# Kernel optimization log

Hardware: AMD Instinct MI355X
Metric: run time of the kernel (lower is better)

Reference implementation:

```python
import jax, jax.numpy as jnp
import numpy as np

MARGIN = 0.075
CONF_THRESHOLD = 0.2


def setup_inputs() -> dict:
    key = jax.random.key(0)
    k1, k2, k3 = jax.random.split(key, 3)
    N, D = 32768, 256
    embeddings = jax.random.normal(k1, (N, D), dtype=jnp.float32)
    tags = jax.random.randint(k2, (N,), 0, 500, dtype=jnp.int64)
    confidences = jax.random.uniform(k3, (N,), dtype=jnp.float32)
    return {"embeddings": embeddings, "tags": tags, "confidences": confidences}


def _safe_sqrt(sq):
    # gradient-safe sqrt: zero at sq<=0 (matches d(0)=0, avoids NaN in vjp)
    pos = sq > 0
    return jnp.where(pos, jnp.sqrt(jnp.where(pos, sq, 1.0)), 0.0)


def _triplet_hard_mining(emb, labels):
    n = emb.shape[0]
    # pairwise euclidean distances (cdist p=2)
    sq_norm = jnp.sum(emb * emb, axis=1)  # [n]
    sq = sq_norm[:, None] + sq_norm[None, :] - 2.0 * (emb @ emb.T)
    dist = _safe_sqrt(jnp.maximum(sq, 0.0))  # [n, n]

    same = labels[:, None] == labels[None, :]
    eye = jnp.eye(n, dtype=bool)
    pos_mask = same & ~eye
    neg_mask = ~same

    inf = jnp.float32(jnp.inf)
    hard_pos = jnp.max(jnp.where(pos_mask, dist, -inf), axis=1)  # [n]
    neg_min = jnp.min(jnp.where(neg_mask, dist, inf), axis=1)    # [n]
    # semi-hard negatives: neg dists strictly greater than hardest positive
    shn_mask = neg_mask & (dist > hard_pos[:, None])
    shn_min = jnp.min(jnp.where(shn_mask, dist, inf), axis=1)
    hard_neg = jnp.where(jnp.isfinite(shn_min), shn_min, neg_min)

    valid = jnp.any(pos_mask, axis=1) & jnp.any(neg_mask, axis=1)
    per_anchor = jax.nn.relu(hard_pos - hard_neg + MARGIN)
    per_anchor = jnp.where(valid, per_anchor, 0.0)
    cnt = jnp.sum(valid.astype(jnp.float32))
    # if no valid anchors (also covers <2 unique labels), loss is 0
    return jnp.where(cnt > 0, jnp.sum(per_anchor) / jnp.maximum(cnt, 1.0), 0.0)


def reference(embeddings, tags, confidences):
    n = embeddings.shape[0]
    top_k = int(CONF_THRESHOLD * n)
    _, idx = jax.lax.top_k(confidences, top_k)
    emb = embeddings[idx]
    labels = tags[idx]
    return _triplet_hard_mining(emb, labels)
```

## Files before the change

### kernel.cpp

```cpp
#include <hip/hip_runtime.h>
#include <math.h>

#define D 256
#define MARGIN 0.075f
#define MAXM 96

typedef __bf16 bf8_t __attribute__((ext_vector_type(8)));
typedef float f4_t __attribute__((ext_vector_type(4)));
typedef unsigned long long ull;

#define AS1 __attribute__((address_space(1)))
#define AS3 __attribute__((address_space(3)))
static __device__ __forceinline__ void gload_lds16(const void* g, void* s) {
    __builtin_amdgcn_global_load_lds((const AS1 unsigned int*)g, (AS3 unsigned int*)s, 16, 0, 0);
}

static __device__ __forceinline__ unsigned short f2bf(float x) {
    unsigned u = __float_as_uint(x);
    unsigned r = (u + 0x7fffu + ((u >> 16) & 1u)) >> 16;
    return (unsigned short)r;
}

static __device__ __forceinline__ float dec_min(unsigned cm) {
    return (cm == 0u) ? __builtin_inff() : __uint_as_float(~cm);
}

static __device__ __forceinline__ float rmin16(float v) {
    int s;
    s = __builtin_amdgcn_update_dpp(__float_as_int(v), __float_as_int(v), 0x101, 0xF, 0xF, false);
    v = fminf(v, __int_as_float(s));
    s = __builtin_amdgcn_update_dpp(__float_as_int(v), __float_as_int(v), 0x102, 0xF, 0xF, false);
    v = fminf(v, __int_as_float(s));
    s = __builtin_amdgcn_update_dpp(__float_as_int(v), __float_as_int(v), 0x104, 0xF, 0xF, false);
    v = fminf(v, __int_as_float(s));
    s = __builtin_amdgcn_update_dpp(__float_as_int(v), __float_as_int(v), 0x108, 0xF, 0xF, false);
    v = fminf(v, __int_as_float(s));
    return v;
}

__global__ void k_hist1(const float* __restrict__ conf, int n,
                        unsigned* __restrict__ hist) {
    int i = blockIdx.x * blockDim.x + threadIdx.x;
    if (i < n) atomicAdd(&hist[__float_as_uint(conf[i]) >> 16], 1u);
}

__global__ __launch_bounds__(1024) void k_scan(const unsigned* __restrict__ hist,
                                               unsigned* __restrict__ ctrl, int ksel) {
    __shared__ unsigned part[1024];
    __shared__ int schunk;
    int t = threadIdx.x;
    unsigned k = (unsigned)ksel;
    unsigned s = 0;
    const uint4* h4 = (const uint4*)(hist + t * 64);
    #pragma unroll
    for (int b = 0; b < 16; b++) { uint4 v = h4[b]; s += v.x + v.y + v.z + v.w; }
    part[t] = s;
    __syncthreads();
    for (int off = 1; off < 1024; off <<= 1) {
        unsigned v = (t + off < 1024) ? part[t + off] : 0u;
        __syncthreads();
        part[t] += v;
        __syncthreads();
    }
    if (part[t] >= k && (t == 1023 || part[t + 1] < k)) schunk = t;
    __syncthreads();
    if (t == 0) {
        int c = schunk;
        unsigned cum = (c == 1023) ? 0u : part[c + 1];
        int bin = 0; unsigned rem = 1;
        for (int b = 63; b >= 0; b--) {
            unsigned h = hist[c * 64 + b];
            if (cum + h >= k) { bin = c * 64 + b; rem = k - cum; break; }
            cum += h;
        }
        ctrl[3] = (unsigned)bin;
        ctrl[1] = k - rem;
        ctrl[2] = rem;
    }
}

__global__ void k_sel(const float* __restrict__ conf, int n,
                      unsigned* __restrict__ ctrl, int* __restrict__ idx_sel,
                      ull* __restrict__ cand) {
    int i = blockIdx.x * blockDim.x + threadIdx.x;
    if (i < n) {
        unsigned u = __float_as_uint(conf[i]);
        unsigned t16 = u >> 16, b16 = ctrl[3];
        if (t16 > b16) {
            unsigned pos = atomicAdd(&ctrl[5], 1u);
            idx_sel[pos] = i;
        } else if (t16 == b16) {
            unsigned pos = atomicAdd(&ctrl[6], 1u);
            cand[pos] = ((ull)u << 32) | (unsigned)i;
        }
    }
}

__global__ __launch_bounds__(256) void k_sel2(const unsigned* __restrict__ ctrl,
                                              const ull* __restrict__ cand,
                                              int* __restrict__ idx_sel) {
    int t = threadIdx.x;
    int M = (int)ctrl[6];
    unsigned need = ctrl[2], cgt = ctrl[1];
    for (int j = t; j < M; j += 256) {
        ull cj = cand[j];
        unsigned uj = (unsigned)(cj >> 32);
        unsigned rank = 0;
        for (int m = 0; m < M; m++) {
            ull cm = cand[m];
            unsigned um = (unsigned)(cm >> 32);
            if (um > uj || (um == uj && cm < cj)) rank++;
        }
        if (rank < need) idx_sel[cgt + rank] = (int)(unsigned)(cj & 0xFFFFFFFFu);
    }
}

__global__ void k_gather(const float* __restrict__ emb, const int* __restrict__ tags,
                         const int* __restrict__ idx_sel, int ksel, int np,
                         unsigned short* __restrict__ ebf, float* __restrict__ sqn,
                         int* __restrict__ lsel, unsigned* __restrict__ labhist,
                         int* __restrict__ members) {
    int j = blockIdx.x;
    int t = threadIdx.x;
    if (j < ksel) {
        int src = idx_sel[j];
        float4 v = *(const float4*)&emb[(size_t)src * D + t * 4];
        ushort4 o;
        o.x = f2bf(v.x); o.y = f2bf(v.y); o.z = f2bf(v.z); o.w = f2bf(v.w);
        *(ushort4*)&ebf[(size_t)j * D + t * 4] = o;
        float s = v.x * v.x + v.y * v.y + v.z * v.z + v.w * v.w;
        for (int off = 32; off > 0; off >>= 1) s += __shfl_down(s, off);
        if (t == 0) {
            int lab = tags[src];
            sqn[j] = s; lsel[j] = lab;
            unsigned slot = atomicAdd(&labhist[lab], 1u);
            if (slot < MAXM) members[lab * MAXM + slot] = j;
        }
    } else {
        ushort4 z = {0, 0, 0, 0};
        *(ushort4*)&ebf[(size_t)j * D + t * 4] = z;
        if (t == 0) { sqn[j] = 0.f; lsel[j] = -1; }
    }
}

__global__ __launch_bounds__(256) void k_hardpos(const unsigned short* __restrict__ ebf,
                                                 const float* __restrict__ sqn,
                                                 const int* __restrict__ members,
                                                 const unsigned* __restrict__ labhist,
                                                 unsigned* __restrict__ hp_g) {
    int L = blockIdx.x;
    int t = threadIdx.x;
    int m = (int)labhist[L];
    if (m > MAXM) m = MAXM;
    if (m < 2) return;

    __shared__ unsigned short rows[MAXM * 256];
    __shared__ float lsqn[MAXM];
    __shared__ unsigned hpl[MAXM];
    __shared__ int ridx[MAXM];

    for (int a = t; a < m; a += 256) {
        int r = members[L * MAXM + a];
        ridx[a] = r; lsqn[a] = sqn[r]; hpl[a] = 0u;
    }
    __syncthreads();
    for (int e = t * 8; e < m * 256; e += 256 * 8) {
        int a = e >> 8, c = e & 255;
        *(uint4*)&rows[a * 256 + c] = *(const uint4*)&ebf[(size_t)ridx[a] * D + c];
    }
    __syncthreads();

    int npair = m * (m - 1) / 2;
    for (int pidx = t; pidx < npair; pidx += 256) {
        int a = 0, rem = pidx;
        while (rem >= m - 1 - a) { rem -= m - 1 - a; a++; }
        int b = a + 1 + rem;
        const unsigned* ra = (const unsigned*)&rows[a * 256];
        const unsigned* rb = (const unsigned*)&rows[b * 256];
        float dot = 0.f;
        #pragma unroll 8
        for (int c = 0; c < 128; c++) {
            unsigned ua = ra[c], ub = rb[c];
            float a0 = __uint_as_float(ua << 16);
            float a1 = __uint_as_float(ua & 0xFFFF0000u);
            float b0 = __uint_as_float(ub << 16);
            float b1 = __uint_as_float(ub & 0xFFFF0000u);
            dot = fmaf(a0, b0, dot);
            dot = fmaf(a1, b1, dot);
        }
        float dsq = fmaxf(lsqn[a] + lsqn[b] - 2.f * dot, 0.f);
        unsigned bits = __float_as_uint(dsq);
        atomicMax(&hpl[a], bits);
        atomicMax(&hpl[b], bits);
    }
    __syncthreads();
    for (int a = t; a < m; a += 256) hp_g[ridx[a]] = hpl[a];
}

__global__ __launch_bounds__(256, 3) void k_fused(const unsigned short* __restrict__ Ebf,
                                                  const float* __restrict__ sqn,
                                                  const int* __restrict__ lsel,
                                                  const unsigned* __restrict__ hp_g,
                                                  unsigned* __restrict__ nm_g,
                                                  unsigned* __restrict__ shn_g,
                                                  int np, int nb, int ksel) {
    int rem = blockIdx.x, bi = 0;
    while (rem >= nb - bi) { rem -= nb - bi; bi++; }
    int bj = bi + rem;
    int i0 = bi * 128, j0 = bj * 128;
    bool diag = (bi == bj);

    __shared__ __align__(16) char smem[32768];
    char* ldsA = smem;
    char* ldsB = smem + 16384;

    int t = threadIdx.x;
    int w = t >> 6, l = t & 63;
    int wm = w & 1, wn = w >> 1;
    int lr = l & 15, lq = l >> 4;
    int r7 = lr & 7, rh = lr >> 3;

    int dr = l >> 3;
    int sg = (l & 7) ^ dr;
    const unsigned short* gA = Ebf + (size_t)(i0 + dr) * D + sg * 8;
    const unsigned short* gB = Ebf + (size_t)(j0 + dr) * D + sg * 8;

    f4_t zero = {0.f, 0.f, 0.f, 0.f};
    f4_t acc[4][4];
    #pragma unroll
    for (int p = 0; p < 4; p++)
        #pragma unroll
        for (int q = 0; q < 4; q++) acc[p][q] = zero;

    for (int k0 = 0; k0 < D; k0 += 64) {
        #pragma unroll
        for (int c = 0; c < 4; c++) {
            int R0 = w * 32 + c * 8;
            gload_lds16(gA + (size_t)R0 * D + k0, ldsA + R0 * 128);
            gload_lds16(gB + (size_t)R0 * D + k0, ldsB + R0 * 128);
        }
        __syncthreads();
        #pragma unroll
        for (int ks8 = 0; ks8 < 8; ks8 += 4) {
            bf8_t a[4], b[4];
            #pragma unroll
            for (int p = 0; p < 4; p++) {
                int off = ((wm * 8 + p * 2 + rh) << 10) + ((r7 * 8 + ((ks8 + lq) ^ r7)) << 4);
                a[p] = *(const bf8_t*)(ldsA + off);
            }
            #pragma unroll
            for (int q = 0; q < 4; q++) {
                int off = ((wn * 8 + q * 2 + rh) << 10) + ((r7 * 8 + ((ks8 + lq) ^ r7)) << 4);
                b[q] = *(const bf8_t*)(ldsB + off);
            }
            #pragma unroll
            for (int p = 0; p < 4; p++)
                #pragma unroll
                for (int q = 0; q < 4; q++)
                    acc[p][q] = __builtin_amdgcn_mfma_f32_16x16x32_bf16(a[p], b[q], acc[p][q], 0, 0, 0);
        }
        __syncthreads();
    }

    float* sqnA = (float*)smem;
    float* sqnB = sqnA + 128;
    int* labA = (int*)(sqnB + 128);
    int* labB = labA + 128;
    float* hpA2 = (float*)(labB + 128);
    float* hpB2 = hpA2 + 128;
    if (t < 128) {
        sqnA[t] = sqn[i0 + t];
        labA[t] = lsel[i0 + t];
        hpA2[t] = __uint_as_float(hp_g[i0 + t]);
    } else {
        int u = t - 128;
        sqnB[u] = sqn[j0 + u];
        labB[u] = lsel[j0 + u];
        hpB2[u] = __uint_as_float(hp_g[j0 + u]);
    }
    __syncthreads();

    const float INF = __builtin_inff();
    float dsq[4][4][4];
    int colL[4], ljv[4];
    #pragma unroll
    for (int q = 0; q < 4; q++) { colL[q] = wn * 64 + q * 16 + lr; ljv[q] = labB[colL[q]]; }
    #pragma unroll
    for (int p = 0; p < 4; p++) {
        #pragma unroll
        for (int r = 0; r < 4; r++) {
            int rowL = wm * 64 + p * 16 + lq * 4 + r;
            int gm = i0 + rowL;
            float smi = sqnA[rowL];
            #pragma unroll
            for (int q = 0; q < 4; q++) {
                int gn = j0 + colL[q];
                float s = fmaxf(smi + sqnB[colL[q]] - 2.f * acc[p][q][r], 0.f);
                dsq[p][q][r] = (gm < ksel && gn < ksel) ? s : INF;
            }
        }
    }

    #pragma unroll
    for (int p = 0; p < 4; p++) {
        #pragma unroll
        for (int r = 0; r < 4; r++) {
            int rowL = wm * 64 + p * 16 + lq * 4 + r;
            int li = labA[rowL];
            float hpr = hpA2[rowL];
            float nmv = INF, smv = INF;
            #pragma unroll
            for (int q = 0; q < 4; q++) {
                float d = dsq[p][q][r];
                if (ljv[q] != li) {
                    nmv = fminf(nmv, d);
                    if (d > hpr) smv = fminf(smv, d);
                }
            }
            nmv = rmin16(nmv);
            smv = rmin16(smv);
            if (lr == 0) {
                if (nmv < INF) atomicMax(&nm_g[i0 + rowL], ~__float_as_uint(nmv));
                if (smv < INF) atomicMax(&shn_g[i0 + rowL], ~__float_as_uint(smv));
            }
        }
    }

    if (!diag) {
        #pragma unroll
        for (int q = 0; q < 4; q++) {
            int lj = ljv[q];
            float hpc = hpB2[colL[q]];
            float nmv = INF, smv = INF;
            #pragma unroll
            for (int p = 0; p < 4; p++)
                #pragma unroll
                for (int r = 0; r < 4; r++) {
                    int rowL = wm * 64 + p * 16 + lq * 4 + r;
                    float d = dsq[p][q][r];
                    if (labA[rowL] != lj) {
                        nmv = fminf(nmv, d);
                        if (d > hpc) smv = fminf(smv, d);
                    }
                }
            nmv = fminf(nmv, __shfl_xor(nmv, 16));
            nmv = fminf(nmv, __shfl_xor(nmv, 32));
            smv = fminf(smv, __shfl_xor(smv, 16));
            smv = fminf(smv, __shfl_xor(smv, 32));
            if (lq == 0) {
                if (nmv < INF) atomicMax(&nm_g[j0 + colL[q]], ~__float_as_uint(nmv));
                if (smv < INF) atomicMax(&shn_g[j0 + colL[q]], ~__float_as_uint(smv));
            }
        }
    }
}

__global__ __launch_bounds__(256) void k_loss(const unsigned* __restrict__ hp,
                                              const unsigned* __restrict__ nm,
                                              const unsigned* __restrict__ shn,
                                              const int* __restrict__ lsel,
                                              const unsigned* __restrict__ labhist,
                                              int ksel, float* __restrict__ fsums,
                                              unsigned* __restrict__ ctrl,
                                              float* __restrict__ out) {
    __shared__ float ssum[256], scnt[256];
    int t = threadIdx.x;
    int i = blockIdx.x * 256 + t;
    float sum = 0.f, cnt = 0.f;
    if (i < ksel) {
        int li = lsel[i];
        unsigned h = labhist[li];
        bool valid = (h >= 2u) && ((unsigned)ksel > h);
        float hp2 = __uint_as_float(hp[i]);
        float nm2 = dec_min(nm[i]);
        float sh2 = dec_min(shn[i]);
        float hn2 = isinf(sh2) ? nm2 : sh2;
        float lv = valid ? fmaxf(sqrtf(hp2) - sqrtf(hn2) + MARGIN, 0.f) : 0.f;
        sum = lv;
        cnt = valid ? 1.f : 0.f;
    }
    ssum[t] = sum; scnt[t] = cnt;
    __syncthreads();
    for (int off = 128; off > 0; off >>= 1) {
        if (t < off) { ssum[t] += ssum[t + off]; scnt[t] += scnt[t + off]; }
        __syncthreads();
    }
    if (t == 0) {
        atomicAdd(&fsums[0], ssum[0]);
        atomicAdd(&fsums[1], scnt[0]);
        __threadfence();
        unsigned done = atomicAdd(&ctrl[7], 1u);
        if (done == gridDim.x - 1) {
            float s = atomicAdd(&fsums[0], 0.f);
            float c = atomicAdd(&fsums[1], 0.f);
            out[0] = (c > 0.f) ? (s / fmaxf(c, 1.f)) : 0.f;
        }
    }
}

__global__ void k_wsfail(float* out, float code) { out[0] = code; }

static inline size_t align_up(size_t x, size_t a) { return (x + a - 1) & ~(a - 1); }

extern "C" void kernel_launch(void* const* d_in, const int* in_sizes, int n_in,
                              void* d_out, int out_size, void* d_ws, size_t ws_size,
                              hipStream_t stream) {
    const float* emb  = (const float*)d_in[0];
    const int*   tags = (const int*)d_in[1];
    const float* conf = (const float*)d_in[2];
    float* out = (float*)d_out;

    int n = in_sizes[2];
    int ksel = (int)(0.2 * (double)n);
    int np = ((ksel + 127) / 128) * 128;
    int nb = np / 128;
    int nlab = 512;

    size_t off = 0;
    size_t o_ctrl = off; off = align_up(off + 32 * sizeof(unsigned), 256);
    size_t o_fs   = off; off = align_up(off + 8 * sizeof(float), 256);
    size_t o_lh   = off; off = align_up(off + (size_t)nlab * 4, 256);
    size_t o_hp   = off; off = align_up(off + (size_t)np * 4, 256);
    size_t o_nm   = off; off = align_up(off + (size_t)np * 4, 256);
    size_t o_shn  = off; off = align_up(off + (size_t)np * 4, 256);
    size_t o_h1   = off; off = align_up(off + 65536 * 4, 256);
    size_t zero_bytes = off;
    size_t o_idx  = off; off = align_up(off + (size_t)ksel * 4, 256);
    size_t o_cand = off; off = align_up(off + (size_t)n * 8, 256);
    size_t o_mem  = off; off = align_up(off + (size_t)nlab * MAXM * 4, 256);
    size_t o_lab  = off; off = align_up(off + (size_t)np * 4, 256);
    size_t o_sqn  = off; off = align_up(off + (size_t)np * 4, 256);
    size_t o_ebf  = off; off = align_up(off + (size_t)np * D * 2, 256);

    if (ws_size < off) {
        k_wsfail<<<1, 1, 0, stream>>>(out, -(float)(ws_size >> 20));
        return;
    }

    char* ws = (char*)d_ws;
    unsigned*       ctrl    = (unsigned*)(ws + o_ctrl);
    float*          fsums   = (float*)(ws + o_fs);
    unsigned*       labhist = (unsigned*)(ws + o_lh);
    unsigned*       hp_g    = (unsigned*)(ws + o_hp);
    unsigned*       nm_g    = (unsigned*)(ws + o_nm);
    unsigned*       shn_g   = (unsigned*)(ws + o_shn);
    unsigned*       h1      = (unsigned*)(ws + o_h1);
    int*            idx_sel = (int*)(ws + o_idx);
    ull*            cand    = (ull*)(ws + o_cand);
    int*            members = (int*)(ws + o_mem);
    int*            lsel    = (int*)(ws + o_lab);
    float*          sqn     = (float*)(ws + o_sqn);
    unsigned short* ebf     = (unsigned short*)(ws + o_ebf);

    hipMemsetAsync(d_ws, 0, zero_bytes, stream);
    k_hist1<<<(n + 255) / 256, 256, 0, stream>>>(conf, n, h1);
    k_scan<<<1, 1024, 0, stream>>>(h1, ctrl, ksel);
    k_sel<<<(n + 255) / 256, 256, 0, stream>>>(conf, n, ctrl, idx_sel, cand);
    k_sel2<<<1, 256, 0, stream>>>(ctrl, cand, idx_sel);
    k_gather<<<np, 64, 0, stream>>>(emb, tags, idx_sel, ksel, np, ebf, sqn, lsel,
                                    labhist, members);
    k_hardpos<<<512, 256, 0, stream>>>(ebf, sqn, members, labhist, hp_g);
    int ntri = nb * (nb + 1) / 2;
    k_fused<<<ntri, 256, 0, stream>>>(ebf, sqn, lsel, hp_g, nm_g, shn_g, np, nb, ksel);
    k_loss<<<(ksel + 255) / 256, 256, 0, stream>>>(hp_g, nm_g, shn_g, lsel, labhist,
                                                   ksel, fsums, ctrl, out);
}
```

Before: 185.9 us.

## Fuse selection kernels via last-block pattern and simplify distance epilogue

Merges the histogram and scan kernels, and the select and rank kernels, into two launches. Each uses a last-block-done atomic counter, so the final block does the serial scan or rank work, and the rank step stages candidates in LDS. The fused distance epilogue now skips the row-norm add and the per-element bound checks by setting padded rows' norm to infinity. It folds the row norm into a per-row threshold and adds it back only at the final atomic. This removes two launches and many VALU ops per tile, at the cost of memory-fence ordering subtleties and a changed padding convention.

Result: slower. 194.4 us (+4.6%).

```diff
diff --git a/kernel.cpp b/kernel.cpp
--- a/kernel.cpp
+++ b/kernel.cpp
@@ -7,6 +7,7 @@
 
 typedef __bf16 bf8_t __attribute__((ext_vector_type(8)));
 typedef float f4_t __attribute__((ext_vector_type(4)));
+typedef int i4_t __attribute__((ext_vector_type(4)));
 typedef unsigned long long ull;
 
 #define AS1 __attribute__((address_space(1)))
@@ -38,76 +39,99 @@
     return v;
 }
 
-__global__ void k_hist1(const float* __restrict__ conf, int n,
-                        unsigned* __restrict__ hist) {
-    int i = blockIdx.x * blockDim.x + threadIdx.x;
-    if (i < n) atomicAdd(&hist[__float_as_uint(conf[i]) >> 16], 1u);
-}
-
-__global__ __launch_bounds__(1024) void k_scan(const unsigned* __restrict__ hist,
-                                               unsigned* __restrict__ ctrl, int ksel) {
-    __shared__ unsigned part[1024];
+__global__ __launch_bounds__(256) void k_histscan(const float* __restrict__ conf,
+                                                  int n, int ksel,
+                                                  unsigned* __restrict__ h1,
+                                                  unsigned* __restrict__ ctrl) {
+    int t = threadIdx.x;
+    int i = blockIdx.x * 256 + t;
+    if (i < n) atomicAdd(&h1[__float_as_uint(conf[i]) >> 16], 1u);
+    __threadfence();
+    __syncthreads();
+    __shared__ unsigned sdone;
+    if (t == 0) sdone = atomicAdd(&ctrl[8], 1u);
+    __syncthreads();
+    if (sdone != gridDim.x - 1) return;
+    __threadfence();
+    __shared__ unsigned part[256], sfx[256];
     __shared__ int schunk;
-    int t = threadIdx.x;
     unsigned k = (unsigned)ksel;
     unsigned s = 0;
-    const uint4* h4 = (const uint4*)(hist + t * 64);
+    const uint4* h4 = (const uint4*)(h1 + t * 256);
     #pragma unroll
-    for (int b = 0; b < 16; b++) { uint4 v = h4[b]; s += v.x + v.y + v.z + v.w; }
+    for (int b = 0; b < 64; b++) { uint4 v = h4[b]; s += v.x + v.y + v.z + v.w; }
     part[t] = s;
     __syncthreads();
-    for (int off = 1; off < 1024; off <<= 1) {
-        unsigned v = (t + off < 1024) ? part[t + off] : 0u;
+    for (int off = 1; off < 256; off <<= 1) {
+        unsigned v = (t + off < 256) ? part[t + off] : 0u;
         __syncthreads();
         part[t] += v;
         __syncthreads();
     }
-    if (part[t] >= k && (t == 1023 || part[t + 1] < k)) schunk = t;
-    __syncthreads();
-    if (t == 0) {
-        int c = schunk;
-        unsigned cum = (c == 1023) ? 0u : part[c + 1];
-        int bin = 0; unsigned rem = 1;
-        for (int b = 63; b >= 0; b--) {
-            unsigned h = hist[c * 64 + b];
-            if (cum + h >= k) { bin = c * 64 + b; rem = k - cum; break; }
-            cum += h;
-        }
-        ctrl[3] = (unsigned)bin;
-        ctrl[1] = k - rem;
-        ctrl[2] = rem;
-    }
-}
-
-__global__ void k_sel(const float* __restrict__ conf, int n,
-                      unsigned* __restrict__ ctrl, int* __restrict__ idx_sel,
-                      ull* __restrict__ cand) {
-    int i = blockIdx.x * blockDim.x + threadIdx.x;
+    if (part[t] >= k && (t == 255 || part[t + 1] < k)) schunk = t;
+    __syncthreads();
+    int c = schunk;
+    unsigned above = (c == 255) ? 0u : part[c + 1];
+    sfx[t] = h1[c * 256 + t];
+    __syncthreads();
+    for (int off = 1; off < 256; off <<= 1) {
+        unsigned v = (t + off < 256) ? sfx[t + off] : 0u;
+        __syncthreads();
+        sfx[t] += v;
+        __syncthreads();
+    }
+    if (above + sfx[t] >= k && (t == 255 || above + sfx[t + 1] < k)) {
+        unsigned gt = above + ((t == 255) ? 0u : sfx[t + 1]);
+        ctrl[3] = (unsigned)(c * 256 + t);
+        ctrl[1] = gt;
+        ctrl[2] = k - gt;
+    }
+}
+
+__global__ __launch_bounds__(256) void k_selrank(const float* __restrict__ conf, int n,
+                                                 unsigned* __restrict__ ctrl,
+                                                 int* __restrict__ idx_sel,
+                                                 ull* __restrict__ cand) {
+    int t = threadIdx.x;
+    int i = blockIdx.x * 256 + t;
+    unsigned b16 = ctrl[3];
     if (i < n) {
         unsigned u = __float_as_uint(conf[i]);
-        unsigned t16 = u >> 16, b16 = ctrl[3];
+        unsigned t16 = u >> 16;
         if (t16 > b16) {
             unsigned pos = atomicAdd(&ctrl[5], 1u);
             idx_sel[pos] = i;
         } else if (t16 == b16) {
             unsigned pos = atomicAdd(&ctrl[6], 1u);
-            cand[pos] = ((ull)u << 32) | (unsigned)i;
-        }
-    }
-}
-
-__global__ __launch_bounds__(256) void k_sel2(const unsigned* __restrict__ ctrl,
-                                              const ull* __restrict__ cand,
-                                              int* __restrict__ idx_sel) {
-    int t = threadIdx.x;
-    int M = (int)ctrl[6];
+            __hip_atomic_store(&cand[pos], ((ull)u << 32) | (unsigned)i,
+                               __ATOMIC_RELAXED, __HIP_MEMORY_SCOPE_AGENT);
+        }
+    }
+    __threadfence();
+    __syncthreads();
+    __shared__ unsigned sdone;
+    if (t == 0) sdone = atomicAdd(&ctrl[9], 1u);
+    __syncthreads();
+    if (sdone != gridDim.x - 1) return;
+    __threadfence();
+
+    __shared__ ull scand[1024];
+    int M = (int)__hip_atomic_load(&ctrl[6], __ATOMIC_RELAXED, __HIP_MEMORY_SCOPE_AGENT);
     unsigned need = ctrl[2], cgt = ctrl[1];
+    bool useLds = (M <= 1024);
+    if (useLds) {
+        for (int m = t; m < M; m += 256)
+            scand[m] = __hip_atomic_load(&cand[m], __ATOMIC_RELAXED, __HIP_MEMORY_SCOPE_AGENT);
+        __syncthreads();
+    }
     for (int j = t; j < M; j += 256) {
-        ull cj = cand[j];
+        ull cj = useLds ? scand[j]
+                        : __hip_atomic_load(&cand[j], __ATOMIC_RELAXED, __HIP_MEMORY_SCOPE_AGENT);
         unsigned uj = (unsigned)(cj >> 32);
         unsigned rank = 0;
         for (int m = 0; m < M; m++) {
-            ull cm = cand[m];
+            ull cm = useLds ? scand[m]
+                            : __hip_atomic_load(&cand[m], __ATOMIC_RELAXED, __HIP_MEMORY_SCOPE_AGENT);
             unsigned um = (unsigned)(cm >> 32);
             if (um > uj || (um == uj && cm < cj)) rank++;
         }
@@ -139,7 +163,7 @@
     } else {
         ushort4 z = {0, 0, 0, 0};
         *(ushort4*)&ebf[(size_t)j * D + t * 4] = z;
-        if (t == 0) { sqn[j] = 0.f; lsel[j] = -1; }
+        if (t == 0) { sqn[j] = __builtin_inff(); lsel[j] = -1; }
     }
 }
 
@@ -266,62 +290,63 @@
     float* sqnB = sqnA + 128;
     int* labA = (int*)(sqnB + 128);
     int* labB = labA + 128;
-    float* hpA2 = (float*)(labB + 128);
-    float* hpB2 = hpA2 + 128;
+    float* thrA = (float*)(labB + 128);
+    float* thrB = thrA + 128;
     if (t < 128) {
-        sqnA[t] = sqn[i0 + t];
-        labA[t] = lsel[i0 + t];
-        hpA2[t] = __uint_as_float(hp_g[i0 + t]);
+        float s = sqn[i0 + t];
+        sqnA[t] = s; labA[t] = lsel[i0 + t];
+        thrA[t] = __uint_as_float(hp_g[i0 + t]) - s;
     } else {
         int u = t - 128;
-        sqnB[u] = sqn[j0 + u];
-        labB[u] = lsel[j0 + u];
-        hpB2[u] = __uint_as_float(hp_g[j0 + u]);
+        float s = sqn[j0 + u];
+        sqnB[u] = s; labB[u] = lsel[j0 + u];
+        thrB[u] = __uint_as_float(hp_g[j0 + u]) - s;
     }
     __syncthreads();
 
     const float INF = __builtin_inff();
-    float dsq[4][4][4];
     int colL[4], ljv[4];
+    float sBq[4], thrBq[4];
     #pragma unroll
-    for (int q = 0; q < 4; q++) { colL[q] = wn * 64 + q * 16 + lr; ljv[q] = labB[colL[q]]; }
+    for (int q = 0; q < 4; q++) {
+        colL[q] = wn * 64 + q * 16 + lr;
+        ljv[q] = labB[colL[q]];
+        sBq[q] = sqnB[colL[q]];
+        thrBq[q] = thrB[colL[q]];
+    }
+    f4_t sqA4[4], thrA4[4];
+    i4_t labA4[4];
+    #pragma unroll
+    for (int p = 0; p < 4; p++) {
+        int rb = wm * 64 + p * 16 + lq * 4;
+        sqA4[p] = *(const f4_t*)&sqnA[rb];
+        thrA4[p] = *(const f4_t*)&thrA[rb];
+        labA4[p] = *(const i4_t*)&labA[rb];
+    }
+
     #pragma unroll
     for (int p = 0; p < 4; p++) {
         #pragma unroll
         for (int r = 0; r < 4; r++) {
-            int rowL = wm * 64 + p * 16 + lq * 4 + r;
-            int gm = i0 + rowL;
-            float smi = sqnA[rowL];
-            #pragma unroll
-            for (int q = 0; q < 4; q++) {
-                int gn = j0 + colL[q];
-                float s = fmaxf(smi + sqnB[colL[q]] - 2.f * acc[p][q][r], 0.f);
-                dsq[p][q][r] = (gm < ksel && gn < ksel) ? s : INF;
-            }
-        }
-    }
-
-    #pragma unroll
-    for (int p = 0; p < 4; p++) {
-        #pragma unroll
-        for (int r = 0; r < 4; r++) {
-            int rowL = wm * 64 + p * 16 + lq * 4 + r;
-            int li = labA[rowL];
-            float hpr = hpA2[rowL];
+            int li = labA4[p][r];
+            float thr = thrA4[p][r];
             float nmv = INF, smv = INF;
             #pragma unroll
             for (int q = 0; q < 4; q++) {
-                float d = dsq[p][q][r];
-                if (ljv[q] != li) {
-                    nmv = fminf(nmv, d);
-                    if (d > hpr) smv = fminf(smv, d);
-                }
+                float v = fmaf(-2.f, acc[p][q][r], sBq[q]);
+                v = (ljv[q] == li) ? INF : v;
+                nmv = fminf(nmv, v);
+                smv = fminf(smv, (v > thr) ? v : INF);
             }
             nmv = rmin16(nmv);
             smv = rmin16(smv);
             if (lr == 0) {
-                if (nmv < INF) atomicMax(&nm_g[i0 + rowL], ~__float_as_uint(nmv));
-                if (smv < INF) atomicMax(&shn_g[i0 + rowL], ~__float_as_uint(smv));
+                int gm = i0 + wm * 64 + p * 16 + lq * 4 + r;
+                float sqi = sqA4[p][r];
+                if (nmv < INF)
+                    atomicMax(&nm_g[gm], ~__float_as_uint(fmaxf(sqi + nmv, 0.f)));
+                if (smv < INF)
+                    atomicMax(&shn_g[gm], ~__float_as_uint(fmaxf(sqi + smv, 0.f)));
             }
         }
     }
@@ -330,26 +355,27 @@
         #pragma unroll
         for (int q = 0; q < 4; q++) {
             int lj = ljv[q];
-            float hpc = hpB2[colL[q]];
+            float thrc = thrBq[q];
             float nmv = INF, smv = INF;
             #pragma unroll
             for (int p = 0; p < 4; p++)
                 #pragma unroll
                 for (int r = 0; r < 4; r++) {
-                    int rowL = wm * 64 + p * 16 + lq * 4 + r;
-                    float d = dsq[p][q][r];
-                    if (labA[rowL] != lj) {
-                        nmv = fminf(nmv, d);
-                        if (d > hpc) smv = fminf(smv, d);
-                    }
+                    float w2 = fmaf(-2.f, acc[p][q][r], sqA4[p][r]);
+                    w2 = (labA4[p][r] == lj) ? INF : w2;
+                    nmv = fminf(nmv, w2);
+                    smv = fminf(smv, (w2 > thrc) ? w2 : INF);
                 }
             nmv = fminf(nmv, __shfl_xor(nmv, 16));
             nmv = fminf(nmv, __shfl_xor(nmv, 32));
             smv = fminf(smv, __shfl_xor(smv, 16));
             smv = fminf(smv, __shfl_xor(smv, 32));
             if (lq == 0) {
-                if (nmv < INF) atomicMax(&nm_g[j0 + colL[q]], ~__float_as_uint(nmv));
-                if (smv < INF) atomicMax(&shn_g[j0 + colL[q]], ~__float_as_uint(smv));
+                int gn = j0 + colL[q];
+                if (nmv < INF)
+                    atomicMax(&nm_g[gn], ~__float_as_uint(fmaxf(sBq[q] + nmv, 0.f)));
+                if (smv < INF)
+                    atomicMax(&shn_g[gn], ~__float_as_uint(fmaxf(sBq[q] + smv, 0.f)));
             }
         }
     }
@@ -453,10 +479,9 @@
     unsigned short* ebf     = (unsigned short*)(ws + o_ebf);
 
     hipMemsetAsync(d_ws, 0, zero_bytes, stream);
-    k_hist1<<<(n + 255) / 256, 256, 0, stream>>>(conf, n, h1);
-    k_scan<<<1, 1024, 0, stream>>>(h1, ctrl, ksel);
-    k_sel<<<(n + 255) / 256, 256, 0, stream>>>(conf, n, ctrl, idx_sel, cand);
-    k_sel2<<<1, 256, 0, stream>>>(ctrl, cand, idx_sel);
+    int selgrid = (n + 255) / 256;
+    k_histscan<<<selgrid, 256, 0, stream>>>(conf, n, ksel, h1, ctrl);
+    k_selrank<<<selgrid, 256, 0, stream>>>(conf, n, ctrl, idx_sel, cand);
     k_gather<<<np, 64, 0, stream>>>(emb, tags, idx_sel, ksel, np, ebf, sqn, lsel,
                                     labhist, members);
     k_hardpos<<<512, 256, 0, stream>>>(ebf, sqn, members, labhist, hp_g);
```
